# Performance work log

Measured on AMD Instinct MI355X. Metric: run time of the kernel, lower is better.

## Reference

```python
import jax, jax.numpy as jnp
import numpy as np

SPARSITY = 0.01

def quantize(weight, s):
    # ternary quantization: (-s, 0, +s); computed under no_grad in torch
    pos = (weight > s).astype(weight.dtype)
    neg = (weight < -s).astype(weight.dtype)
    return (pos - neg) * s

def setup_inputs() -> dict:
    key = jax.random.key(0)
    k1, k2, k3 = jax.random.split(key, 3)
    B, N, Din, Dout = 8, 2048, 256, 256
    x = jax.random.normal(k1, (B, N, Din), dtype=jnp.float32)
    adj = jax.random.uniform(k2, (B, N, N), dtype=jnp.float32)
    # xavier_uniform_ over (in_dim, out_dim)
    limit = float(np.sqrt(6.0 / (Din + Dout)))
    weight = jax.random.uniform(k3, (Din, Dout), dtype=jnp.float32, minval=-limit, maxval=limit)
    bias = jnp.zeros((Dout,), dtype=jnp.float32)
    return {"x": x, "adj": adj, "weight": weight, "bias": bias}

def reference(x, adj, weight, bias):
    dw = quantize(weight, SPARSITY)          # [Din, Dout] ternary * s
    support = jnp.einsum('bni,io->bno', x, dw)   # [B, N, Dout]
    out = jnp.einsum('bnm,bmo->bno', adj, support) + bias
    return jax.nn.relu(out)
```

## Files before the change

### kernel.cpp

```cpp
#include <hip/hip_runtime.h>
#include <stdint.h>

typedef __attribute__((ext_vector_type(8))) short short8;
typedef __attribute__((ext_vector_type(4))) float f32x4;

static_assert(sizeof(short8) == 16, "frag size");

__device__ __forceinline__ uint16_t f2bf(float f) {
  uint32_t u = __builtin_bit_cast(uint32_t, f);
  u += 0x7fffu + ((u >> 16) & 1u);
  return (uint16_t)(u >> 16);
}

__device__ __forceinline__ void gload_lds16(const void* g, void* lds_wave_base) {
  __builtin_amdgcn_global_load_lds(
      (__attribute__((address_space(1))) void*)(void*)(g),
      (__attribute__((address_space(3))) void*)(lds_wave_base),
      16, 0, 0);
}

__global__ __launch_bounds__(256) void quant_kernel(const float* __restrict__ w,
                                                    uint16_t* __restrict__ dwT) {
  const int o = blockIdx.x;
  const int i = threadIdx.x;
  const float v = w[i * 256 + o];
  const float t = (v > 0.01f) ? 1.0f : ((v < -0.01f) ? -1.0f : 0.0f);
  dwT[o * 256 + (i ^ ((o & 7) << 3))] = f2bf(t);
}

#define K1_A 0
#define K1_B 32768

__global__ __launch_bounds__(256) void support_kernel(const float* __restrict__ x,
                                                      const uint16_t* __restrict__ dwT,
                                                      uint16_t* __restrict__ spt) {
  __shared__ __align__(16) unsigned char smem[32768 + 8192];
  const int t = threadIdx.x;
  const int lane = t & 63;
  const int w = t >> 6;
  const int wbase = w * 64;
  const int n0 = blockIdx.x * 64;
  const int r = lane & 15, q = lane >> 4, e = lane & 7;

  f32x4 acc[4][4] = {};

  for (int k0 = 0; k0 < 256; k0 += 64) {
#pragma unroll
    for (int j = 0; j < 8; ++j) {
      const int idx = j * 256 + t;
      const int row = idx >> 3, c = idx & 7;
      gload_lds16(dwT + (size_t)row * 256 + k0 + c * 8,
                  smem + K1_A + (size_t)(j * 256 + wbase) * 16);
    }
#pragma unroll
    for (int it = 0; it < 4; ++it) {
      const int row = (t >> 4) + it * 16;
      const int c4 = t & 15;
      const float4 v = *(const float4*)(x + (size_t)(n0 + row) * 256 + k0 + c4 * 4);
      const uint32_t lo = (uint32_t)f2bf(v.x) | ((uint32_t)f2bf(v.y) << 16);
      const uint32_t hi = (uint32_t)f2bf(v.z) | ((uint32_t)f2bf(v.w) << 16);
      const int chunk = c4 >> 1, half = c4 & 1;
      *(uint2*)(smem + K1_B + row * 128 + ((chunk ^ (row & 7)) << 4) + half * 8) =
          make_uint2(lo, hi);
    }
    __syncthreads();
#pragma unroll
    for (int h = 0; h < 2; ++h) {
      short8 av[4], bv[4];
      const int pc = ((h * 4 + q) ^ e) << 4;
#pragma unroll
      for (int mi = 0; mi < 4; ++mi)
        av[mi] = *(const short8*)(smem + K1_A + (wbase + 16 * mi + r) * 128 + pc);
#pragma unroll
      for (int ni = 0; ni < 4; ++ni)
        bv[ni] = *(const short8*)(smem + K1_B + (16 * ni + r) * 128 + pc);
#pragma unroll
      for (int mi = 0; mi < 4; ++mi)
#pragma unroll
        for (int ni = 0; ni < 4; ++ni)
          acc[mi][ni] = __builtin_amdgcn_mfma_f32_16x16x32_bf16(av[mi], bv[ni],
                                                                acc[mi][ni], 0, 0, 0);
    }
    __syncthreads();
  }
#pragma unroll
  for (int mi = 0; mi < 4; ++mi)
#pragma unroll
    for (int reg = 0; reg < 4; ++reg) {
      const int o = wbase + 16 * mi + q * 4 + reg;
      const int sw = (o & 7) << 3;
#pragma unroll
      for (int ni = 0; ni < 4; ++ni) {
        const int n = n0 + 16 * ni + r;
        spt[(size_t)o * 16384 + (n ^ sw)] = f2bf(acc[mi][ni][reg] * 0.01f);
      }
    }
}

#define KB_A 0
#define KB_B 9216

__global__ __launch_bounds__(256) void gcn_main_kernel(const float* __restrict__ adj,
                                                       const uint16_t* __restrict__ spt,
                                                       const float* __restrict__ bias,
                                                       float* __restrict__ out) {
  __shared__ __align__(16) unsigned char smem[9216 + 32768];
  const int t = threadIdx.x;
  const int lane = t & 63;
  const int w = t >> 6;
  const int wbase = w * 64;
  const int bb = blockIdx.x & 7;
  const int n0 = (blockIdx.x >> 3) * 64;
  const float* adjb = adj + (size_t)bb * 2048 * 2048;
  const int r = lane & 15, q = lane >> 4, e = lane & 7;

  f32x4 acc[4][4] = {};

  for (int k0 = 0; k0 < 2048; k0 += 64) {
#pragma unroll
    for (int it = 0; it < 4; ++it) {
      const int row = (t >> 4) + it * 16;
      const int c4 = t & 15;
      const float4 v = *(const float4*)(adjb + (size_t)(n0 + row) * 2048 + k0 + c4 * 4);
      const uint32_t lo = (uint32_t)f2bf(v.x) | ((uint32_t)f2bf(v.y) << 16);
      const uint32_t hi = (uint32_t)f2bf(v.z) | ((uint32_t)f2bf(v.w) << 16);
      *(uint2*)(smem + KB_A + row * 144 + c4 * 8) = make_uint2(lo, hi);
    }
#pragma unroll
    for (int j = 0; j < 8; ++j) {
      const int idx = j * 256 + t;
      const int row = idx >> 3, c = idx & 7;
      gload_lds16(spt + (size_t)row * 16384 + bb * 2048 + k0 + c * 8,
                  smem + KB_B + (size_t)(j * 256 + wbase) * 16);
    }
    __syncthreads();
#pragma unroll
    for (int h = 0; h < 2; ++h) {
      short8 av[4], bv[4];
      const int pc = ((h * 4 + q) ^ e) << 4;
#pragma unroll
      for (int mi = 0; mi < 4; ++mi)
        av[mi] = *(const short8*)(smem + KB_A + (16 * mi + r) * 144 + h * 64 + q * 16);
#pragma unroll
      for (int ni = 0; ni < 4; ++ni)
        bv[ni] = *(const short8*)(smem + KB_B + (wbase + 16 * ni + r) * 128 + pc);
#pragma unroll
      for (int mi = 0; mi < 4; ++mi)
#pragma unroll
        for (int ni = 0; ni < 4; ++ni)
          acc[mi][ni] = __builtin_amdgcn_mfma_f32_16x16x32_bf16(av[mi], bv[ni],
                                                                acc[mi][ni], 0, 0, 0);
    }
    __syncthreads();
  }
#pragma unroll
  for (int ni = 0; ni < 4; ++ni) {
    const int o = wbase + 16 * ni + r;
    const float bs = bias[o];
#pragma unroll
    for (int mi = 0; mi < 4; ++mi)
#pragma unroll
      for (int reg = 0; reg < 4; ++reg) {
        const int n = n0 + 16 * mi + q * 4 + reg;
        const float val = acc[mi][ni][reg] + bs;
        out[((size_t)bb * 2048 + n) * 256 + o] = fmaxf(val, 0.0f);
      }
  }
}

extern "C" void kernel_launch(void* const* d_in, const int* in_sizes, int n_in,
                              void* d_out, int out_size, void* d_ws, size_t ws_size,
                              hipStream_t stream) {
  const float* x      = (const float*)d_in[0];
  const float* adj    = (const float*)d_in[1];
  const float* weight = (const float*)d_in[2];
  const float* bias   = (const float*)d_in[3];
  float* out = (float*)d_out;

  uint16_t* dwT = (uint16_t*)d_ws;
  uint16_t* spt = (uint16_t*)((char*)d_ws + 131072);

  hipLaunchKernelGGL(quant_kernel,    dim3(256), dim3(256), 0, stream, weight, dwT);
  hipLaunchKernelGGL(support_kernel,  dim3(256), dim3(256), 0, stream, x, dwT, spt);
  hipLaunchKernelGGL(gcn_main_kernel, dim3(256), dim3(256), 0, stream, adj, spt, bias, out);
}
```

Baseline: 240.5 us.

## Pre-convert adj to bf16 and stream both GEMM operands via direct LDS loads

Adds a separate kernel that converts adj to a swizzled bf16 copy in workspace, so the main GEMM can load both operands with global_load_lds instead of converting fp32 in registers. Both GEMM kernels are retiled to 128x64 output tiles with 512 blocks for more parallelism. The support kernel now stages its output through LDS for coalesced stores. The cost is an extra full pass over adj and each adj tile being reread by four output-column blocks.

```diff
diff --git a/kernel.cpp b/kernel.cpp
--- a/kernel.cpp
+++ b/kernel.cpp
@@ -19,63 +19,78 @@
       16, 0, 0);
 }
 
+
 __global__ __launch_bounds__(256) void quant_kernel(const float* __restrict__ w,
                                                     uint16_t* __restrict__ dwT) {
-  const int o = blockIdx.x;
-  const int i = threadIdx.x;
+  const int o = blockIdx.x, i = threadIdx.x;
   const float v = w[i * 256 + o];
   const float t = (v > 0.01f) ? 1.0f : ((v < -0.01f) ? -1.0f : 0.0f);
   dwT[o * 256 + (i ^ ((o & 7) << 3))] = f2bf(t);
 }
 
-#define K1_A 0
-#define K1_B 32768
+__global__ __launch_bounds__(256) void adjcvt_kernel(const float* __restrict__ adj,
+                                                     uint16_t* __restrict__ adjB) {
+  const int g = blockIdx.x;
+  const int c = threadIdx.x;
+  const float* p = adj + (size_t)g * 2048 + c * 8;
+  const float4 v0 = *(const float4*)p;
+  const float4 v1 = *(const float4*)(p + 4);
+  uint4 u;
+  u.x = (uint32_t)f2bf(v0.x) | ((uint32_t)f2bf(v0.y) << 16);
+  u.y = (uint32_t)f2bf(v0.z) | ((uint32_t)f2bf(v0.w) << 16);
+  u.z = (uint32_t)f2bf(v1.x) | ((uint32_t)f2bf(v1.y) << 16);
+  u.w = (uint32_t)f2bf(v1.z) | ((uint32_t)f2bf(v1.w) << 16);
+  const int phys = (c & ~7) | ((c & 7) ^ (g & 7));
+  *(uint4*)(adjB + (size_t)g * 2048 + phys * 8) = u;
+}
+
+#define SB_A 0
+#define SB_B 16384
 
 __global__ __launch_bounds__(256) void support_kernel(const float* __restrict__ x,
                                                       const uint16_t* __restrict__ dwT,
                                                       uint16_t* __restrict__ spt) {
-  __shared__ __align__(16) unsigned char smem[32768 + 8192];
-  const int t = threadIdx.x;
-  const int lane = t & 63;
-  const int w = t >> 6;
-  const int wbase = w * 64;
-  const int n0 = blockIdx.x * 64;
-  const int r = lane & 15, q = lane >> 4, e = lane & 7;
-
-  f32x4 acc[4][4] = {};
+  __shared__ __align__(16) unsigned char smem[24576];
+  const int t = threadIdx.x, lane = t & 63, w = t >> 6;
+  const int r = lane & 15, q = lane >> 4;
+  const int g0 = (blockIdx.x & 127) * 128;
+  const int o0 = (blockIdx.x >> 7) * 64;
+
+  f32x4 acc[2][4] = {};
 
   for (int k0 = 0; k0 < 256; k0 += 64) {
 #pragma unroll
-    for (int j = 0; j < 8; ++j) {
-      const int idx = j * 256 + t;
-      const int row = idx >> 3, c = idx & 7;
-      gload_lds16(dwT + (size_t)row * 256 + k0 + c * 8,
-                  smem + K1_A + (size_t)(j * 256 + wbase) * 16);
-    }
-#pragma unroll
     for (int it = 0; it < 4; ++it) {
-      const int row = (t >> 4) + it * 16;
-      const int c4 = t & 15;
-      const float4 v = *(const float4*)(x + (size_t)(n0 + row) * 256 + k0 + c4 * 4);
-      const uint32_t lo = (uint32_t)f2bf(v.x) | ((uint32_t)f2bf(v.y) << 16);
-      const uint32_t hi = (uint32_t)f2bf(v.z) | ((uint32_t)f2bf(v.w) << 16);
-      const int chunk = c4 >> 1, half = c4 & 1;
-      *(uint2*)(smem + K1_B + row * 128 + ((chunk ^ (row & 7)) << 4) + half * 8) =
-          make_uint2(lo, hi);
+      const int id = it * 256 + t, row = id >> 3, c = id & 7;
+      const float* p = x + (size_t)(g0 + row) * 256 + k0 + c * 8;
+      const float4 v0 = *(const float4*)p;
+      const float4 v1 = *(const float4*)(p + 4);
+      uint4 u;
+      u.x = (uint32_t)f2bf(v0.x) | ((uint32_t)f2bf(v0.y) << 16);
+      u.y = (uint32_t)f2bf(v0.z) | ((uint32_t)f2bf(v0.w) << 16);
+      u.z = (uint32_t)f2bf(v1.x) | ((uint32_t)f2bf(v1.y) << 16);
+      u.w = (uint32_t)f2bf(v1.z) | ((uint32_t)f2bf(v1.w) << 16);
+      *(uint4*)(smem + SB_A + row * 128 + ((c ^ (row & 7)) << 4)) = u;
+    }
+#pragma unroll
+    for (int j = 0; j < 2; ++j) {
+      const int id = j * 256 + t, row = id >> 3, c = id & 7;
+      gload_lds16(dwT + (size_t)(o0 + row) * 256 + k0 + c * 8,
+                  smem + SB_B + (size_t)(j * 256 + w * 64) * 16);
     }
     __syncthreads();
 #pragma unroll
     for (int h = 0; h < 2; ++h) {
-      short8 av[4], bv[4];
-      const int pc = ((h * 4 + q) ^ e) << 4;
-#pragma unroll
-      for (int mi = 0; mi < 4; ++mi)
-        av[mi] = *(const short8*)(smem + K1_A + (wbase + 16 * mi + r) * 128 + pc);
+      short8 av[2], bv[4];
+      const int pc = (((h * 4 + q) ^ (r & 7)) << 4);
+#pragma unroll
+      for (int mi = 0; mi < 2; ++mi)
+        av[mi] = *(const short8*)(smem + SB_A + (32 * w + 16 * mi + r) * 128 + pc);
 #pragma unroll
       for (int ni = 0; ni < 4; ++ni)
-        bv[ni] = *(const short8*)(smem + K1_B + (16 * ni + r) * 128 + pc);
-#pragma unroll
-      for (int mi = 0; mi < 4; ++mi)
+        bv[ni] = *(const short8*)(smem + SB_B + (16 * ni + r) * 128 + pc);
+#pragma unroll
+      for (int mi = 0; mi < 2; ++mi)
 #pragma unroll
         for (int ni = 0; ni < 4; ++ni)
           acc[mi][ni] = __builtin_amdgcn_mfma_f32_16x16x32_bf16(av[mi], bv[ni],
@@ -84,68 +99,70 @@
     __syncthreads();
   }
 #pragma unroll
-  for (int mi = 0; mi < 4; ++mi)
-#pragma unroll
-    for (int reg = 0; reg < 4; ++reg) {
-      const int o = wbase + 16 * mi + q * 4 + reg;
-      const int sw = (o & 7) << 3;
-#pragma unroll
-      for (int ni = 0; ni < 4; ++ni) {
-        const int n = n0 + 16 * ni + r;
-        spt[(size_t)o * 16384 + (n ^ sw)] = f2bf(acc[mi][ni][reg] * 0.01f);
+  for (int ni = 0; ni < 4; ++ni) {
+    const int ol = 16 * ni + r;
+#pragma unroll
+    for (int mi = 0; mi < 2; ++mi)
+#pragma unroll
+      for (int reg = 0; reg < 4; ++reg) {
+        const int gl = 32 * w + 16 * mi + 4 * q + reg;
+        const int gsw = gl ^ ((ol & 7) << 3);
+        *(uint16_t*)(smem + (ol * 128 + gsw) * 2) = f2bf(acc[mi][ni][reg] * 0.01f);
       }
-    }
-}
-
-#define KB_A 0
-#define KB_B 9216
-
-__global__ __launch_bounds__(256) void gcn_main_kernel(const float* __restrict__ adj,
+  }
+  __syncthreads();
+#pragma unroll
+  for (int it = 0; it < 4; ++it) {
+    const int id = it * 256 + t, row = id >> 4, cc = id & 15;
+    const uint4 u = *(const uint4*)(smem + (row * 128 + cc * 8) * 2);
+    *(uint4*)(spt + (size_t)(o0 + row) * 16384 + g0 + cc * 8) = u;
+  }
+}
+
+#define MB_A 0
+#define MB_B 16384
+
+__global__ __launch_bounds__(256) void gcn_main_kernel(const uint16_t* __restrict__ adjB,
                                                        const uint16_t* __restrict__ spt,
                                                        const float* __restrict__ bias,
                                                        float* __restrict__ out) {
-  __shared__ __align__(16) unsigned char smem[9216 + 32768];
-  const int t = threadIdx.x;
-  const int lane = t & 63;
-  const int w = t >> 6;
-  const int wbase = w * 64;
+  __shared__ __align__(16) unsigned char smem[24576];
+  const int t = threadIdx.x, lane = t & 63, w = t >> 6;
+  const int r = lane & 15, q = lane >> 4;
   const int bb = blockIdx.x & 7;
-  const int n0 = (blockIdx.x >> 3) * 64;
-  const float* adjb = adj + (size_t)bb * 2048 * 2048;
-  const int r = lane & 15, q = lane >> 4, e = lane & 7;
-
-  f32x4 acc[4][4] = {};
+  const int n0 = ((blockIdx.x >> 3) & 15) * 128;
+  const int o0 = (blockIdx.x >> 7) * 64;
+  const uint16_t* adjb = adjB + ((size_t)bb * 2048 + n0) * 2048;
+  const uint16_t* sptb = spt + (size_t)bb * 2048;
+
+  f32x4 acc[2][4] = {};
 
   for (int k0 = 0; k0 < 2048; k0 += 64) {
 #pragma unroll
-    for (int it = 0; it < 4; ++it) {
-      const int row = (t >> 4) + it * 16;
-      const int c4 = t & 15;
-      const float4 v = *(const float4*)(adjb + (size_t)(n0 + row) * 2048 + k0 + c4 * 4);
-      const uint32_t lo = (uint32_t)f2bf(v.x) | ((uint32_t)f2bf(v.y) << 16);
-      const uint32_t hi = (uint32_t)f2bf(v.z) | ((uint32_t)f2bf(v.w) << 16);
-      *(uint2*)(smem + KB_A + row * 144 + c4 * 8) = make_uint2(lo, hi);
-    }
-#pragma unroll
-    for (int j = 0; j < 8; ++j) {
-      const int idx = j * 256 + t;
-      const int row = idx >> 3, c = idx & 7;
-      gload_lds16(spt + (size_t)row * 16384 + bb * 2048 + k0 + c * 8,
-                  smem + KB_B + (size_t)(j * 256 + wbase) * 16);
+    for (int j = 0; j < 4; ++j) {
+      const int id = j * 256 + t, row = id >> 3, c = id & 7;
+      gload_lds16(adjb + (size_t)row * 2048 + k0 + c * 8,
+                  smem + MB_A + (size_t)(j * 256 + w * 64) * 16);
+    }
+#pragma unroll
+    for (int j = 0; j < 2; ++j) {
+      const int id = j * 256 + t, row = id >> 3, c = id & 7;
+      gload_lds16(sptb + (size_t)(o0 + row) * 16384 + k0 + c * 8,
+                  smem + MB_B + (size_t)(j * 256 + w * 64) * 16);
     }
     __syncthreads();
 #pragma unroll
     for (int h = 0; h < 2; ++h) {
-      short8 av[4], bv[4];
-      const int pc = ((h * 4 + q) ^ e) << 4;
-#pragma unroll
-      for (int mi = 0; mi < 4; ++mi)
-        av[mi] = *(const short8*)(smem + KB_A + (16 * mi + r) * 144 + h * 64 + q * 16);
+      short8 av[2], bv[4];
+      const int pc = (((h * 4 + q) ^ (r & 7)) << 4);
+#pragma unroll
+      for (int mi = 0; mi < 2; ++mi)
+        av[mi] = *(const short8*)(smem + MB_A + (32 * w + 16 * mi + r) * 128 + pc);
 #pragma unroll
       for (int ni = 0; ni < 4; ++ni)
-        bv[ni] = *(const short8*)(smem + KB_B + (wbase + 16 * ni + r) * 128 + pc);
-#pragma unroll
-      for (int mi = 0; mi < 4; ++mi)
+        bv[ni] = *(const short8*)(smem + MB_B + (16 * ni + r) * 128 + pc);
+#pragma unroll
+      for (int mi = 0; mi < 2; ++mi)
 #pragma unroll
         for (int ni = 0; ni < 4; ++ni)
           acc[mi][ni] = __builtin_amdgcn_mfma_f32_16x16x32_bf16(av[mi], bv[ni],
@@ -155,15 +172,14 @@
   }
 #pragma unroll
   for (int ni = 0; ni < 4; ++ni) {
-    const int o = wbase + 16 * ni + r;
+    const int o = o0 + 16 * ni + r;
     const float bs = bias[o];
 #pragma unroll
-    for (int mi = 0; mi < 4; ++mi)
+    for (int mi = 0; mi < 2; ++mi)
 #pragma unroll
       for (int reg = 0; reg < 4; ++reg) {
-        const int n = n0 + 16 * mi + q * 4 + reg;
-        const float val = acc[mi][ni][reg] + bs;
-        out[((size_t)bb * 2048 + n) * 256 + o] = fmaxf(val, 0.0f);
+        const int n = n0 + 32 * w + 16 * mi + 4 * q + reg;
+        out[((size_t)bb * 2048 + n) * 256 + o] = fmaxf(acc[mi][ni][reg] + bs, 0.0f);
       }
   }
 }
@@ -177,10 +193,12 @@
   const float* bias   = (const float*)d_in[3];
   float* out = (float*)d_out;
 
-  uint16_t* dwT = (uint16_t*)d_ws;
-  uint16_t* spt = (uint16_t*)((char*)d_ws + 131072);
-
-  hipLaunchKernelGGL(quant_kernel,    dim3(256), dim3(256), 0, stream, weight, dwT);
-  hipLaunchKernelGGL(support_kernel,  dim3(256), dim3(256), 0, stream, x, dwT, spt);
-  hipLaunchKernelGGL(gcn_main_kernel, dim3(256), dim3(256), 0, stream, adj, spt, bias, out);
-}
+  uint16_t* dwT  = (uint16_t*)d_ws;
+  uint16_t* spt  = (uint16_t*)((char*)d_ws + (131072));
+  uint16_t* adjB = (uint16_t*)((char*)d_ws + (131072 + 8388608));
+
+  hipLaunchKernelGGL(quant_kernel,    dim3(256),   dim3(256), 0, stream, weight, dwT);
+  hipLaunchKernelGGL(adjcvt_kernel,   dim3(16384), dim3(256), 0, stream, adj, adjB);
+  hipLaunchKernelGGL(support_kernel,  dim3(512),   dim3(256), 0, stream, x, dwT, spt);
+  hipLaunchKernelGGL(gcn_main_kernel, dim3(512),   dim3(256), 0, stream, adjB, spt, bias, out);
+}
```

Measured after the change: 255.2 us. +6.1%, slower.
